# Optimization experiments

Measured on AMD Instinct MI355X. Metric: run time of the kernel, lower is better.

## Reference

```python
import jax, jax.numpy as jnp
import numpy as np

IN_FEATURES = 100000
OUT_FEATURES = 100000
NNZ = 1600000
BATCH = 64


def setup_inputs() -> dict:
    key = jax.random.key(0)
    k1, k2, k3, k4, k5 = jax.random.split(key, 5)
    x = jax.random.normal(k1, (BATCH, IN_FEATURES), dtype=jnp.float32)
    values = jax.random.normal(k2, (NNZ,), dtype=jnp.float32)
    bias = jax.random.normal(k3, (OUT_FEATURES,), dtype=jnp.float32)
    # torch COO is coalesced -> row indices sorted (rows = dst of transposed matrix)
    rows = jnp.sort(jax.random.randint(k4, (NNZ,), 0, OUT_FEATURES, dtype=jnp.int64))
    cols = jax.random.randint(k5, (NNZ,), 0, IN_FEATURES, dtype=jnp.int64)
    return {"x": x, "values": values, "bias": bias, "rows": rows, "cols": cols}


def reference(x, values, bias, rows, cols):
    # out = x @ conn  <=>  out.T = conn_T @ x.T, conn_T given in COO (rows=dst, cols=src)
    # gather source activations along edges: (nnz, B)
    contrib = x[:, cols].T * values[:, None]
    # scatter-add into destinations: (out_features, B)
    out_t = jax.ops.segment_sum(contrib, rows, num_segments=OUT_FEATURES,
                                indices_are_sorted=True)
    return out_t.T + bias  # (B, out_features)
```

## Files before the change

kernel.cpp:

```cpp
#include <hip/hip_runtime.h>
#include <hip/hip_fp16.h>

#define IN_F   100000
#define OUT_F  100000
#define NNZ_N  1600000

#define TC 256
__global__ __launch_bounds__(256) void k_x_to_half_t(
    const float* __restrict__ x, __half* __restrict__ xh) {
    __shared__ unsigned tile[TC][33];
    const int i0 = blockIdx.x * TC;
    const int t  = threadIdx.x;
    const int colr = i0 + t;

    if (colr < IN_F) {
        #pragma unroll 4
        for (int p = 0; p < 32; ++p) {
            const float a = x[(size_t)(2 * p)     * IN_F + colr];
            const float b = x[(size_t)(2 * p + 1) * IN_F + colr];
            const __half2 h = __floats2half2_rn(a, b);
            tile[t][p] = *reinterpret_cast<const unsigned*>(&h);
        }
    }
    __syncthreads();

    const int u  = t & 31;
    const int c8 = t >> 5;
    unsigned* xhu = reinterpret_cast<unsigned*>(xh);
    for (int cc = c8; cc < TC; cc += 8) {
        const int col = i0 + cc;
        if (col < IN_F)
            xhu[(size_t)col * 32 + u] = tile[cc][u];
    }
}

__global__ __launch_bounds__(256) void k_rowstart(
    const int* __restrict__ rows, int* __restrict__ rstart) {
    const int r = blockIdx.x * 256 + threadIdx.x;
    if (r > OUT_F) return;
    int lo = 0, hi = NNZ_N;
    while (lo < hi) {
        const int mid = (lo + hi) >> 1;
        if (rows[mid] < r) lo = mid + 1; else hi = mid;
    }
    rstart[r] = lo;
}

__device__ __forceinline__ float2 h2f(unsigned u) {
    const __half2 h = *reinterpret_cast<const __half2*>(&u);
    return __half22float2(h);
}

__global__ __launch_bounds__(512, 8) void k_spmm_h(
    const __half* __restrict__ xh,
    const float*  __restrict__ vals,
    const int*    __restrict__ cols,
    const int*    __restrict__ rstart_g,
    const float*  __restrict__ bias,
    float* __restrict__ out) {
    __shared__ int   rs[65];
    __shared__ float tile[64][65];
    const int r0   = blockIdx.x * 64;
    const int t    = threadIdx.x;
    const int lane = t & 63;
    const int w    = t >> 6;

    if (t < 65) {
        int idx = r0 + t; if (idx > OUT_F) idx = OUT_F;
        rs[t] = rstart_g[idx];
    }
    __syncthreads();

    const int g   = lane >> 4;
    const int sub = lane & 15;
    const __half* xb = xh + (sub << 2);

    #pragma unroll
    for (int r = 0; r < 2; ++r) {
        const int lj = (w << 3) + (r << 2) + g;
        const int s = rs[lj];
        const int e = rs[lj + 1];
        float4 acc = {0.f, 0.f, 0.f, 0.f};

        for (int base = s; base < e; base += 4) {
            const int e1 = e - 1;
            const int i1 = (base + 1 < e) ? base + 1 : e1;
            const int i2 = (base + 2 < e) ? base + 2 : e1;
            const int i3 = (base + 3 < e) ? base + 3 : e1;
            const int c0 = cols[base], c1 = cols[i1], c2 = cols[i2], c3 = cols[i3];
            const float v0 = vals[base];
            float v1 = vals[i1]; if (base + 1 >= e) v1 = 0.f;
            float v2 = vals[i2]; if (base + 2 >= e) v2 = 0.f;
            float v3 = vals[i3]; if (base + 3 >= e) v3 = 0.f;
            const uint2 u0 = *(const uint2*)(xb + ((size_t)c0 << 6));
            const uint2 u1 = *(const uint2*)(xb + ((size_t)c1 << 6));
            const uint2 u2 = *(const uint2*)(xb + ((size_t)c2 << 6));
            const uint2 u3 = *(const uint2*)(xb + ((size_t)c3 << 6));
            float2 f;
            f = h2f(u0.x); acc.x = fmaf(v0, f.x, acc.x); acc.y = fmaf(v0, f.y, acc.y);
            f = h2f(u0.y); acc.z = fmaf(v0, f.x, acc.z); acc.w = fmaf(v0, f.y, acc.w);
            f = h2f(u1.x); acc.x = fmaf(v1, f.x, acc.x); acc.y = fmaf(v1, f.y, acc.y);
            f = h2f(u1.y); acc.z = fmaf(v1, f.x, acc.z); acc.w = fmaf(v1, f.y, acc.w);
            f = h2f(u2.x); acc.x = fmaf(v2, f.x, acc.x); acc.y = fmaf(v2, f.y, acc.y);
            f = h2f(u2.y); acc.z = fmaf(v2, f.x, acc.z); acc.w = fmaf(v2, f.y, acc.w);
            f = h2f(u3.x); acc.x = fmaf(v3, f.x, acc.x); acc.y = fmaf(v3, f.y, acc.y);
            f = h2f(u3.y); acc.z = fmaf(v3, f.x, acc.z); acc.w = fmaf(v3, f.y, acc.w);
        }
        const int co = sub << 2;
        tile[lj][co + 0] = acc.x;
        tile[lj][co + 1] = acc.y;
        tile[lj][co + 2] = acc.z;
        tile[lj][co + 3] = acc.w;
    }
    __syncthreads();

    const int rc = r0 + lane;
    if (rc < OUT_F) {
        const float bv = bias[rc];
        for (int bb = w; bb < 64; bb += 8)
            out[(size_t)bb * OUT_F + rc] = tile[lane][bb] + bv;
    }
}

__global__ __launch_bounds__(256) void k_spmm_fallback(
    const float* __restrict__ x,
    const float* __restrict__ vals,
    const int*   __restrict__ rows,
    const int*   __restrict__ cols,
    const float* __restrict__ bias,
    float* __restrict__ out) {
    __shared__ int   rstart[65];
    __shared__ float tile[64][65];
    const int r0   = blockIdx.x * 64;
    const int t    = threadIdx.x;
    const int lane = t & 63;
    const int w    = t >> 6;
    if (t < 65) {
        const int target = r0 + t;
        int lo = 0, hi = NNZ_N;
        while (lo < hi) {
            const int mid = (lo + hi) >> 1;
            if (rows[mid] < target) lo = mid + 1; else hi = mid;
        }
        rstart[t] = lo;
    }
    __syncthreads();
    for (int j = w; j < 64; j += 4) {
        const int s = rstart[j], e = rstart[j + 1];
        float acc = 0.f;
        const size_t base = (size_t)lane * IN_F;
        for (int idx = s; idx < e; ++idx)
            acc = fmaf(vals[idx], x[base + cols[idx]], acc);
        tile[j][lane] = acc;
    }
    __syncthreads();
    const int c = lane;
    if (r0 + c < OUT_F) {
        const float bv = bias[r0 + c];
        for (int bb = w; bb < 64; bb += 4)
            out[(size_t)bb * OUT_F + (r0 + c)] = tile[c][bb] + bv;
    }
}

extern "C" void kernel_launch(void* const* d_in, const int* in_sizes, int n_in,
                              void* d_out, int out_size, void* d_ws, size_t ws_size,
                              hipStream_t stream) {
    const float* x      = (const float*)d_in[0];
    const float* values = (const float*)d_in[1];
    const float* bias   = (const float*)d_in[2];
    const int*   rows   = (const int*)d_in[3];
    const int*   cols   = (const int*)d_in[4];
    float*       out    = (float*)d_out;

    const size_t xh_bytes = (size_t)IN_F * 64 * sizeof(__half);
    const size_t rs_off   = (xh_bytes + 255) & ~(size_t)255;
    const size_t need     = rs_off + (size_t)(OUT_F + 1) * sizeof(int);

    const int row_blocks = (OUT_F + 63) / 64;
    const int tc_blocks  = (IN_F + TC - 1) / TC;
    const int rs_blocks  = (OUT_F + 1 + 255) / 256;

    if (ws_size >= need) {
        __half* xh     = (__half*)d_ws;
        int*    rstart = (int*)((char*)d_ws + rs_off);
        k_x_to_half_t<<<tc_blocks, 256, 0, stream>>>(x, xh);
        k_rowstart<<<rs_blocks, 256, 0, stream>>>(rows, rstart);
        k_spmm_h<<<row_blocks, 512, 0, stream>>>(xh, values, cols, rstart, bias, out);
    } else {
        k_spmm_fallback<<<row_blocks, 256, 0, stream>>>(x, values, rows, cols, bias, out);
    }
}
```

Measured before the change: 142.7 us.

## Split batch into four slices with per-slice SpMM passes for cache locality

The half-precision transposed activations are now stored in four batch slices of 16 columns each, 32 bytes per input feature. The SpMM runs as four passes, one per slice, so each pass gathers from a 3.2 MB table that fits in cache better than the previous 12.8 MB one. The row-start computation changes from a per-row binary search to a per-nonzero boundary scan. In exchange, cols and vals are reread four times, there are extra kernel launches, and each thread now processes one row with only 2 batch values, which means fewer loads in flight per nonzero.

After: 176.7 us. +23.8%, slower.

```diff
diff --git a/kernel.cpp b/kernel.cpp
--- a/kernel.cpp
+++ b/kernel.cpp
@@ -4,17 +4,18 @@
 #define IN_F   100000
 #define OUT_F  100000
 #define NNZ_N  1600000
+#define NSLICE 4
+#define TC     256
 
-#define TC 256
-__global__ __launch_bounds__(256) void k_x_to_half_t(
-    const float* __restrict__ x, __half* __restrict__ xh) {
+__global__ __launch_bounds__(256) void k_transpose_sliced(
+    const float* __restrict__ x, unsigned* __restrict__ xh) {
     __shared__ unsigned tile[TC][33];
     const int i0 = blockIdx.x * TC;
     const int t  = threadIdx.x;
     const int colr = i0 + t;
 
     if (colr < IN_F) {
-        #pragma unroll 4
+        #pragma unroll 8
         for (int p = 0; p < 32; ++p) {
             const float a = x[(size_t)(2 * p)     * IN_F + colr];
             const float b = x[(size_t)(2 * p + 1) * IN_F + colr];
@@ -24,26 +25,26 @@
     }
     __syncthreads();
 
-    const int u  = t & 31;
-    const int c8 = t >> 5;
-    unsigned* xhu = reinterpret_cast<unsigned*>(xh);
-    for (int cc = c8; cc < TC; cc += 8) {
-        const int col = i0 + cc;
-        if (col < IN_F)
-            xhu[(size_t)col * 32 + u] = tile[cc][u];
+    const int u  = t & 7;
+    const int c0 = t >> 3;
+    for (int s = 0; s < NSLICE; ++s) {
+        for (int cc = c0; cc < TC; cc += 32) {
+            const int col = i0 + cc;
+            if (col < IN_F)
+                xh[((size_t)s * IN_F + col) * 8 + u] = tile[cc][s * 8 + u];
+        }
     }
 }
 
-__global__ __launch_bounds__(256) void k_rowstart(
+__global__ __launch_bounds__(256) void k_rowstart_scan(
     const int* __restrict__ rows, int* __restrict__ rstart) {
-    const int r = blockIdx.x * 256 + threadIdx.x;
-    if (r > OUT_F) return;
-    int lo = 0, hi = NNZ_N;
-    while (lo < hi) {
-        const int mid = (lo + hi) >> 1;
-        if (rows[mid] < r) lo = mid + 1; else hi = mid;
-    }
-    rstart[r] = lo;
+    const int e = blockIdx.x * 256 + threadIdx.x;
+    if (e >= NNZ_N) return;
+    const int cur  = rows[e];
+    const int prev = (e == 0) ? -1 : rows[e - 1];
+    for (int r = prev + 1; r <= cur; ++r) rstart[r] = e;
+    if (e == NNZ_N - 1)
+        for (int r = cur + 1; r <= OUT_F; ++r) rstart[r] = NNZ_N;
 }
 
 __device__ __forceinline__ float2 h2f(unsigned u) {
@@ -51,15 +52,15 @@
     return __half22float2(h);
 }
 
-__global__ __launch_bounds__(512, 8) void k_spmm_h(
-    const __half* __restrict__ xh,
-    const float*  __restrict__ vals,
-    const int*    __restrict__ cols,
-    const int*    __restrict__ rstart_g,
-    const float*  __restrict__ bias,
-    float* __restrict__ out) {
+__global__ __launch_bounds__(512, 8) void k_spmm_pass(
+    const unsigned* __restrict__ xs,
+    const float*    __restrict__ vals,
+    const int*      __restrict__ cols,
+    const int*      __restrict__ rstart_g,
+    const float*    __restrict__ bias,
+    float* __restrict__ out, int b0) {
     __shared__ int   rs[65];
-    __shared__ float tile[64][65];
+    __shared__ float tile[64][17];
     const int r0   = blockIdx.x * 64;
     const int t    = threadIdx.x;
     const int lane = t & 63;
@@ -71,54 +72,43 @@
     }
     __syncthreads();
 
-    const int g   = lane >> 4;
-    const int sub = lane & 15;
-    const __half* xb = xh + (sub << 2);
+    const int g   = lane >> 3;
+    const int sub = lane & 7;
+    const int lj  = (w << 3) + g;
+    const int s   = rs[lj];
+    const int e   = rs[lj + 1];
+    const unsigned* xb = xs + sub;
 
-    #pragma unroll
-    for (int r = 0; r < 2; ++r) {
-        const int lj = (w << 3) + (r << 2) + g;
-        const int s = rs[lj];
-        const int e = rs[lj + 1];
-        float4 acc = {0.f, 0.f, 0.f, 0.f};
-
-        for (int base = s; base < e; base += 4) {
-            const int e1 = e - 1;
-            const int i1 = (base + 1 < e) ? base + 1 : e1;
-            const int i2 = (base + 2 < e) ? base + 2 : e1;
-            const int i3 = (base + 3 < e) ? base + 3 : e1;
-            const int c0 = cols[base], c1 = cols[i1], c2 = cols[i2], c3 = cols[i3];
-            const float v0 = vals[base];
-            float v1 = vals[i1]; if (base + 1 >= e) v1 = 0.f;
-            float v2 = vals[i2]; if (base + 2 >= e) v2 = 0.f;
-            float v3 = vals[i3]; if (base + 3 >= e) v3 = 0.f;
-            const uint2 u0 = *(const uint2*)(xb + ((size_t)c0 << 6));
-            const uint2 u1 = *(const uint2*)(xb + ((size_t)c1 << 6));
-            const uint2 u2 = *(const uint2*)(xb + ((size_t)c2 << 6));
-            const uint2 u3 = *(const uint2*)(xb + ((size_t)c3 << 6));
-            float2 f;
-            f = h2f(u0.x); acc.x = fmaf(v0, f.x, acc.x); acc.y = fmaf(v0, f.y, acc.y);
-            f = h2f(u0.y); acc.z = fmaf(v0, f.x, acc.z); acc.w = fmaf(v0, f.y, acc.w);
-            f = h2f(u1.x); acc.x = fmaf(v1, f.x, acc.x); acc.y = fmaf(v1, f.y, acc.y);
-            f = h2f(u1.y); acc.z = fmaf(v1, f.x, acc.z); acc.w = fmaf(v1, f.y, acc.w);
-            f = h2f(u2.x); acc.x = fmaf(v2, f.x, acc.x); acc.y = fmaf(v2, f.y, acc.y);
-            f = h2f(u2.y); acc.z = fmaf(v2, f.x, acc.z); acc.w = fmaf(v2, f.y, acc.w);
-            f = h2f(u3.x); acc.x = fmaf(v3, f.x, acc.x); acc.y = fmaf(v3, f.y, acc.y);
-            f = h2f(u3.y); acc.z = fmaf(v3, f.x, acc.z); acc.w = fmaf(v3, f.y, acc.w);
-        }
-        const int co = sub << 2;
-        tile[lj][co + 0] = acc.x;
-        tile[lj][co + 1] = acc.y;
-        tile[lj][co + 2] = acc.z;
-        tile[lj][co + 3] = acc.w;
+    float2 acc = {0.f, 0.f};
+    for (int base = s; base < e; base += 4) {
+        const int e1 = e - 1;
+        const int i1 = (base + 1 < e) ? base + 1 : e1;
+        const int i2 = (base + 2 < e) ? base + 2 : e1;
+        const int i3 = (base + 3 < e) ? base + 3 : e1;
+        const int c0 = cols[base], c1 = cols[i1], c2 = cols[i2], c3 = cols[i3];
+        const float v0 = vals[base];
+        float v1 = vals[i1]; if (base + 1 >= e) v1 = 0.f;
+        float v2 = vals[i2]; if (base + 2 >= e) v2 = 0.f;
+        float v3 = vals[i3]; if (base + 3 >= e) v3 = 0.f;
+        const unsigned u0 = xb[(size_t)c0 << 3];
+        const unsigned u1 = xb[(size_t)c1 << 3];
+        const unsigned u2 = xb[(size_t)c2 << 3];
+        const unsigned u3 = xb[(size_t)c3 << 3];
+        float2 f;
+        f = h2f(u0); acc.x = fmaf(v0, f.x, acc.x); acc.y = fmaf(v0, f.y, acc.y);
+        f = h2f(u1); acc.x = fmaf(v1, f.x, acc.x); acc.y = fmaf(v1, f.y, acc.y);
+        f = h2f(u2); acc.x = fmaf(v2, f.x, acc.x); acc.y = fmaf(v2, f.y, acc.y);
+        f = h2f(u3); acc.x = fmaf(v3, f.x, acc.x); acc.y = fmaf(v3, f.y, acc.y);
     }
+    tile[lj][2 * sub]     = acc.x;
+    tile[lj][2 * sub + 1] = acc.y;
     __syncthreads();
 
     const int rc = r0 + lane;
     if (rc < OUT_F) {
         const float bv = bias[rc];
-        for (int bb = w; bb < 64; bb += 8)
-            out[(size_t)bb * OUT_F + rc] = tile[lane][bb] + bv;
+        for (int bb = w; bb < 16; bb += 8)
+            out[(size_t)(b0 + bb) * OUT_F + rc] = tile[lane][bb] + bv;
     }
 }
 
@@ -172,20 +162,24 @@
     const int*   cols   = (const int*)d_in[4];
     float*       out    = (float*)d_out;
 
-    const size_t xh_bytes = (size_t)IN_F * 64 * sizeof(__half);
+    const size_t xh_bytes = (size_t)NSLICE * IN_F * 8 * sizeof(unsigned);
     const size_t rs_off   = (xh_bytes + 255) & ~(size_t)255;
     const size_t need     = rs_off + (size_t)(OUT_F + 1) * sizeof(int);
 
     const int row_blocks = (OUT_F + 63) / 64;
     const int tc_blocks  = (IN_F + TC - 1) / TC;
-    const int rs_blocks  = (OUT_F + 1 + 255) / 256;
+    const int sc_blocks  = (NNZ_N + 255) / 256;
 
     if (ws_size >= need) {
-        __half* xh     = (__half*)d_ws;
-        int*    rstart = (int*)((char*)d_ws + rs_off);
-        k_x_to_half_t<<<tc_blocks, 256, 0, stream>>>(x, xh);
-        k_rowstart<<<rs_blocks, 256, 0, stream>>>(rows, rstart);
-        k_spmm_h<<<row_blocks, 512, 0, stream>>>(xh, values, cols, rstart, bias, out);
+        unsigned* xh     = (unsigned*)d_ws;
+        int*      rstart = (int*)((char*)d_ws + rs_off);
+        k_transpose_sliced<<<tc_blocks, 256, 0, stream>>>(x, xh);
+        k_rowstart_scan<<<sc_blocks, 256, 0, stream>>>(rows, rstart);
+        for (int s = 0; s < NSLICE; ++s) {
+            const unsigned* xs = xh + (size_t)s * IN_F * 8;
+            k_spmm_pass<<<row_blocks, 512, 0, stream>>>(
+                xs, values, cols, rstart, bias, out, s * 16);
+        }
     } else {
         k_spmm_fallback<<<row_blocks, 256, 0, stream>>>(x, values, rows, cols, bias, out);
     }
```
